# Kernel optimization log

Measured on AMD Instinct MI355X. Metric: run time of the kernel, lower is better.

The kernel has to match this reference:

```python
import jax, jax.numpy as jnp
import numpy as np

H = 12          # num_heads
E = 768         # key_dim
LORA_SCALE = 32.0 / 4.0  # scale / R
NEG = -1e9


def setup_inputs() -> dict:
    key = jax.random.key(0)
    ks = jax.random.split(key, 8)
    B, L = 2, 2048
    return {
        "x": jax.random.normal(ks[0], (B, L, E), jnp.float32),
        "w_in": jax.random.normal(ks[1], (E, 3 * E), jnp.float32) * 0.02,
        "b_in": jnp.zeros((3 * E,), jnp.float32),
        "A_in": jax.random.normal(ks[2], (4, 3 * E), jnp.float32) * 0.02,
        "B_in": jax.random.normal(ks[3], (E, 4), jnp.float32) * 0.02,
        "w_out": jax.random.normal(ks[4], (E, E), jnp.float32) * 0.02,
        "b_out": jnp.zeros((E,), jnp.float32),
        "A_out": jax.random.normal(ks[5], (4, E), jnp.float32) * 0.02,
        "B_out": jax.random.normal(ks[6], (E, 4), jnp.float32) * 0.02,
    }


def reference(x, w_in, b_in, A_in, B_in, w_out, b_out, A_out, B_out):
    Bb, L, _ = x.shape
    D = E // H
    # LoRA-adapted input projection: w + (scale/R) * B @ A
    w1 = w_in + LORA_SCALE * (B_in @ A_in)          # [E, 3E]
    c = jnp.einsum('ble,eo->blo', x, w1) + b_in      # [B, L, 3E]
    q, k, v = jnp.split(c, 3, axis=2)
    # split heads -> [B, H, L, D]
    def heads(t):
        return t.reshape(Bb, L, H, D).transpose(0, 2, 1, 3)
    q, k, v = heads(q), heads(k), heads(v)
    # attention scores (no 1/sqrt(d): scale=False in module defaults)
    w = jnp.einsum('bhqd,bhkd->bhqk', q, k)          # [B, H, L, L]
    band = jnp.tril(jnp.ones((L, L), jnp.float32))   # causal band
    w = w * band + NEG * (1.0 - band)
    w = jax.nn.softmax(w, axis=-1)
    a = jnp.einsum('bhqk,bhkd->bhqd', w, v)          # [B, H, L, D]
    a = a.transpose(0, 2, 1, 3).reshape(Bb, L, E)    # merge heads
    w2 = w_out + LORA_SCALE * (B_out @ A_out)        # [E, E]
    return jnp.einsum('ble,eo->blo', a, w2) + b_out
```

## Files before the change

### kernel.cpp

```cpp
#include <hip/hip_runtime.h>
#include <hip/hip_bf16.h>

#define BB 2
#define LL 2048
#define EE 768
#define HH 12
#define DD 64
#define N3 2304
#define TOK 4096
#define LOG2E 1.4426950408889634f

typedef __attribute__((ext_vector_type(8))) short short8;
typedef __attribute__((ext_vector_type(4))) short s16x4;
typedef __attribute__((ext_vector_type(4))) float f32x4;
typedef __attribute__((ext_vector_type(4))) unsigned int uix4;
typedef unsigned int uint_t;
typedef unsigned short ushort_t;

__device__ __forceinline__ f32x4 mfma16(short8 a, short8 b, f32x4 c) {
  return __builtin_amdgcn_mfma_f32_16x16x32_bf16(a, b, c, 0, 0, 0);
}
__device__ __forceinline__ f32x4 mfma16k16(s16x4 a, s16x4 b, f32x4 c) {
  return __builtin_amdgcn_mfma_f32_16x16x16bf16_1k(a, b, c, 0, 0, 0);
}

__device__ __forceinline__ ushort_t bf16bits(float f) {
  __hip_bfloat16 h = __float2bfloat16(f);
  return *reinterpret_cast<ushort_t*>(&h);
}

__device__ __forceinline__ float bits2f(ushort_t u) {
  union { uint_t u; float f; } cv;
  cv.u = ((uint_t)u) << 16;
  return cv.f;
}

__device__ __forceinline__ void stage64(const __hip_bfloat16* gbase, int ldg,
                                        short* lds, int tid) {
  const int wave = tid >> 6, lane = tid & 63;
#pragma unroll
  for (int c = 0; c < 4; ++c) {
    int off = c * 4096 + wave * 1024 + lane * 16;
    int row = off >> 7;
    int cs  = (off & 127) >> 4;
    int cc  = cs ^ (row & 7);
    __builtin_amdgcn_global_load_lds(
        (const __attribute__((address_space(1))) void*)((const short*)gbase + (size_t)row * ldg + cc * 8),
        (__attribute__((address_space(3))) void*)(lds + c * 2048 + wave * 512),
        16, 0, 0);
  }
}

__device__ __forceinline__ void stage128(const __hip_bfloat16* gbase, int ldg,
                                         short* lds, int tid) {
  const int wave = tid >> 6, lane = tid & 63;
#pragma unroll
  for (int c = 0; c < 4; ++c) {
    int off = c * 4096 + wave * 1024 + lane * 16;
    int row = off >> 8;
    int cs  = (off & 255) >> 4;
    int cc  = cs ^ (row & 7);
    __builtin_amdgcn_global_load_lds(
        (const __attribute__((address_space(1))) void*)((const short*)gbase + (size_t)row * ldg + cc * 8),
        (__attribute__((address_space(3))) void*)(lds + c * 2048 + wave * 512),
        16, 0, 0);
  }
}

__device__ __forceinline__ short8 frag64(const short* lds, int row, int chunk) {
  return *(const short8*)(lds + row * 64 + (chunk ^ (row & 7)) * 8);
}

__global__ void prep_kernel(const float* __restrict__ x, const float* __restrict__ w_in,
                            const float* __restrict__ A_in, const float* __restrict__ B_in,
                            const float* __restrict__ w_out, const float* __restrict__ A_out,
                            const float* __restrict__ B_out,
                            __hip_bfloat16* __restrict__ xb, __hip_bfloat16* __restrict__ w1T,
                            __hip_bfloat16* __restrict__ w2T) {
  __shared__ float tile[32][33];
  const int bid = blockIdx.x, t = threadIdx.x;
  if (bid < 2304) {
    const float *W, *Am, *Bm;
    __hip_bfloat16* out;
    int N, tx, ty;
    if (bid < 1728) { W = w_in;  Am = A_in;  Bm = B_in;  out = w1T; N = N3; tx = bid % 72; ty = bid / 72; }
    else { int jj = bid - 1728; W = w_out; Am = A_out; Bm = B_out; out = w2T; N = EE; tx = jj % 24; ty = jj / 24; }
    const int e0 = ty * 32, o0 = tx * 32;
    const int r = t >> 5, col = t & 31;
#pragma unroll
    for (int i = 0; i < 4; ++i)
      tile[r + i * 8][col] = W[(size_t)(e0 + r + i * 8) * N + (o0 + col)];
    __syncthreads();
    const int e = e0 + col;
    const float b0 = Bm[e * 4 + 0], b1 = Bm[e * 4 + 1], b2 = Bm[e * 4 + 2], b3 = Bm[e * 4 + 3];
#pragma unroll
    for (int i = 0; i < 4; ++i) {
      const int o = o0 + r + i * 8;
      float acc = b0 * Am[o] + b1 * Am[N + o] + b2 * Am[2 * N + o] + b3 * Am[3 * N + o];
      out[(size_t)o * EE + e] = __float2bfloat16(tile[col][r + i * 8] + 8.0f * acc);
    }
  } else {
    const int j = bid - 2304;
    const float* src = x + (size_t)j * 4096 + t * 16;
    short* dst = (short*)xb + (size_t)j * 4096 + t * 16;
#pragma unroll
    for (int half = 0; half < 2; ++half) {
      float4 a = ((const float4*)src)[half * 2];
      float4 b = ((const float4*)src)[half * 2 + 1];
      short8 v;
      v[0] = (short)bf16bits(a.x); v[1] = (short)bf16bits(a.y);
      v[2] = (short)bf16bits(a.z); v[3] = (short)bf16bits(a.w);
      v[4] = (short)bf16bits(b.x); v[5] = (short)bf16bits(b.y);
      v[6] = (short)bf16bits(b.z); v[7] = (short)bf16bits(b.w);
      ((short8*)dst)[half] = v;
    }
  }
}

template<bool F32OUT, bool QSCALE>
__global__ __launch_bounds__(256, 2) void gemm_bt(const __hip_bfloat16* __restrict__ A,
                                                  const __hip_bfloat16* __restrict__ BT,
                                                  const float* __restrict__ bias,
                                                  void* __restrict__ outp,
                                                  int M, int N, int K) {
  __shared__ __align__(16) short Al[128 * 64];
  __shared__ __align__(16) short Bl[128 * 64];
  const int tid = threadIdx.x, lane = tid & 63, wave = tid >> 6;
  const int quad = lane >> 4, c16 = lane & 15;
  const int n0 = blockIdx.x * 128, m0 = blockIdx.y * 128;
  const int msub = (wave & 1) * 64, nsub = (wave >> 1) * 64;
  f32x4 acc[4][4] = {};
  for (int k0 = 0; k0 < K; k0 += 64) {
    __syncthreads();
    stage64(A + (size_t)m0 * K + k0, K, Al, tid);
    stage64(BT + (size_t)n0 * K + k0, K, Bl, tid);
    __syncthreads();
#pragma unroll
    for (int ks = 0; ks < 2; ++ks) {
      short8 af[4], bfr[4];
#pragma unroll
      for (int i = 0; i < 4; ++i) {
        af[i]  = frag64(Al, msub + i * 16 + c16, ks * 4 + quad);
        bfr[i] = frag64(Bl, nsub + i * 16 + c16, ks * 4 + quad);
      }
#pragma unroll
      for (int mi = 0; mi < 4; ++mi)
#pragma unroll
        for (int ni = 0; ni < 4; ++ni)
          acc[mi][ni] = mfma16(af[mi], bfr[ni], acc[mi][ni]);
    }
  }
#pragma unroll
  for (int ni = 0; ni < 4; ++ni) {
    int n = n0 + nsub + ni * 16 + c16;
    float bv = bias[n];
    float sc = (QSCALE && n < EE) ? LOG2E : 1.0f;
#pragma unroll
    for (int mi = 0; mi < 4; ++mi) {
      int row0 = m0 + msub + mi * 16 + quad * 4;
#pragma unroll
      for (int r = 0; r < 4; ++r) {
        float v = (acc[mi][ni][r] + bv) * sc;
        if (F32OUT) ((float*)outp)[(size_t)(row0 + r) * N + n] = v;
        else ((__hip_bfloat16*)outp)[(size_t)(row0 + r) * N + n] = __float2bfloat16(v);
      }
    }
  }
}

__global__ void vtrans_kernel(const __hip_bfloat16* __restrict__ qkv,
                              __hip_bfloat16* __restrict__ vT) {
  const int tid = threadIdx.x, lane = tid & 63, wave = tid >> 6;
  const int blk = blockIdx.x;
  const int bh = blk >> 6, lt = blk & 63;
  const int b = bh / HH, h = bh % HH;
  const int l0 = lt * 32 + wave * 8;
  const int i = lane >> 3, o = lane & 7;
  const short* src = (const short*)qkv + (size_t)(b * LL + l0 + i) * N3 + 2 * EE + h * DD + o * 8;
  uix4 u = *(const uix4*)src;
  {
    uix4 ov;
#pragma unroll
    for (int k = 0; k < 4; ++k) ov[k] = (uint_t)__shfl_xor((int)u[k], 8);
#pragma unroll
    for (int k = 0; k < 4; ++k)
      u[k] = ((i & 1) == 0) ? ((u[k] & 0xFFFFu) | (ov[k] << 16))
                            : ((ov[k] >> 16) | (u[k] & 0xFFFF0000u));
  }
  {
    uix4 ov;
#pragma unroll
    for (int k = 0; k < 4; ++k) ov[k] = (uint_t)__shfl_xor((int)u[k], 16);
    uint_t a0 = ((i & 2) == 0) ? u[0] : ov[1];
    uint_t a1 = ((i & 2) == 0) ? ov[0] : u[1];
    uint_t a2 = ((i & 2) == 0) ? u[2] : ov[3];
    uint_t a3 = ((i & 2) == 0) ? ov[2] : u[3];
    u[0] = a0; u[1] = a1; u[2] = a2; u[3] = a3;
  }
  {
    uix4 ov;
#pragma unroll
    for (int k = 0; k < 4; ++k) ov[k] = (uint_t)__shfl_xor((int)u[k], 32);
    uint_t a0 = ((i & 4) == 0) ? u[0] : ov[2];
    uint_t a1 = ((i & 4) == 0) ? u[1] : ov[3];
    uint_t a2 = ((i & 4) == 0) ? ov[0] : u[2];
    uint_t a3 = ((i & 4) == 0) ? ov[1] : u[3];
    u[0] = a0; u[1] = a1; u[2] = a2; u[3] = a3;
  }
  short* dst = (short*)vT + (size_t)((b * HH + h) * DD + o * 8 + i) * LL + l0;
  *(uix4*)dst = u;
}

#define SLOT_BYTES 16896
union pk4 { uint_t u[2]; s16x4 s4; };

__global__ __launch_bounds__(256, 4) void attn_kernel(const __hip_bfloat16* __restrict__ qkv,
                                                      const __hip_bfloat16* __restrict__ vT,
                                                      char* __restrict__ Opart) {
  __shared__ __align__(16) short Kl[128 * 64];
  __shared__ __align__(16) short Vl[64 * 128];
  const int tid = threadIdx.x, lane = tid & 63, wave = tid >> 6;
  const int quad = lane >> 4, c16 = lane & 15;
  const int bid = blockIdx.x;
  const int bh = bid % 24;
  const int j = bid / 24;
  int qt, cch;
  if (j < 8)       { qt = 8 + j;  cch = 0; }
  else if (j < 16) { qt = 23 - j; cch = 1; }
  else             { qt = 23 - j; cch = 0; }
  const int b = bh / HH, h = bh % HH;
  const int q0 = qt * 128;
  const int qw = q0 + wave * 32;
  const int ks = cch * 1024;
  const int ke = min(q0 + 128, ks + 1024);
  short8 qfA[2], qfB[2];
  {
    const short* qra = (const short*)qkv + (size_t)(b * LL + qw + c16) * N3 + h * DD;
    qfA[0] = *(const short8*)(qra + quad * 8);
    qfA[1] = *(const short8*)(qra + 32 + quad * 8);
    const short* qrb = qra + 16 * N3;
    qfB[0] = *(const short8*)(qrb + quad * 8);
    qfB[1] = *(const short8*)(qrb + 32 + quad * 8);
  }
  float lA = 0.f, lB = 0.f;
  f32x4 oA[4] = {}, oB[4] = {};
  const int vsub = (quad & 1) * 4;
  const int cxor = (c16 & 7);
  for (int k0 = ks; k0 < ke; k0 += 128) {
    __syncthreads();
    stage64(qkv + (size_t)(b * LL + k0) * N3 + EE + h * DD, N3, Kl, tid);
    stage128(vT + (size_t)((b * HH + h) * DD) * LL + k0, LL, Vl, tid);
    __syncthreads();
    int nlimB = (qw + 31 - k0) / 16 + 1; if (nlimB > 8) nlimB = 8;
    int nlimA = (qw + 15 - k0) / 16 + 1; if (nlimA > 8) nlimA = 8;
#pragma unroll
    for (int nt = 0; nt < 8; ++nt) {
      if (nt < nlimB) {
        const short* krow = Kl + (nt * 16 + c16) * 64;
        const int kc0 = (quad ^ cxor) * 8;
        short8 kf0 = *(const short8*)(krow + kc0);
        short8 kf1 = *(const short8*)(krow + (kc0 ^ 32));
        const int kb = k0 + nt * 16 + quad * 4;
        const bool diag = (k0 + nt * 16 + 15 > qw + 16);
        f32x4 sB = {};
        sB = mfma16(kf0, qfB[0], sB);
        sB = mfma16(kf1, qfB[1], sB);
        if (diag) {
          const int q = qw + 16 + c16;
#pragma unroll
          for (int r = 0; r < 4; ++r)
            if (kb + r > q) sB[r] = -1e9f;
        }
        pk4 pB;
        {
          float p0 = exp2f(sB[0]), p1 = exp2f(sB[1]);
          float p2 = exp2f(sB[2]), p3 = exp2f(sB[3]);
          lB += (p0 + p1) + (p2 + p3);
          pB.u[0] = (uint_t)bf16bits(p0) | ((uint_t)bf16bits(p1) << 16);
          pB.u[1] = (uint_t)bf16bits(p2) | ((uint_t)bf16bits(p3) << 16);
        }
        const bool doA = (nt < nlimA);
        pk4 pA;
        if (doA) {
          f32x4 sA = {};
          sA = mfma16(kf0, qfA[0], sA);
          sA = mfma16(kf1, qfA[1], sA);
          if (k0 + nt * 16 + 15 > qw) {
            const int q = qw + c16;
#pragma unroll
            for (int r = 0; r < 4; ++r)
              if (kb + r > q) sA[r] = -1e9f;
          }
          float p0 = exp2f(sA[0]), p1 = exp2f(sA[1]);
          float p2 = exp2f(sA[2]), p3 = exp2f(sA[3]);
          lA += (p0 + p1) + (p2 + p3);
          pA.u[0] = (uint_t)bf16bits(p0) | ((uint_t)bf16bits(p1) << 16);
          pA.u[1] = (uint_t)bf16bits(p2) | ((uint_t)bf16bits(p3) << 16);
        }
        const int cg = nt * 2 + (quad >> 1);
        const short* vbase = Vl + c16 * 128 + ((cg ^ cxor) * 8 + vsub);
#pragma unroll
        for (int dt = 0; dt < 4; ++dt) {
          s16x4 vf = *(const s16x4*)(vbase + dt * 2048);
          oB[dt] = mfma16k16(vf, pB.s4, oB[dt]);
          if (doA) oA[dt] = mfma16k16(vf, pA.s4, oA[dt]);
        }
      }
    }
  }
  lA += __shfl_xor(lA, 16); lA += __shfl_xor(lA, 32);
  lB += __shfl_xor(lB, 16); lB += __shfl_xor(lB, 32);
  char* op = Opart + (size_t)((bh * 16 + qt) * 2 + cch) * SLOT_BYTES;
  float* lout = (float*)(op + 16384);
  __syncthreads();
  if (quad == 0) {
    lout[wave * 32 + c16] = lA;
    lout[wave * 32 + 16 + c16] = lB;
  }
  short* reg = Kl + wave * 1152;
#pragma unroll
  for (int hh = 0; hh < 2; ++hh) {
#pragma unroll
    for (int dt = 0; dt < 4; ++dt) {
      f32x4 o = hh ? oB[dt] : oA[dt];
      uint_t w0 = (uint_t)bf16bits(o[0]) | ((uint_t)bf16bits(o[1]) << 16);
      uint_t w1 = (uint_t)bf16bits(o[2]) | ((uint_t)bf16bits(o[3]) << 16);
      uint_t* p = (uint_t*)(reg + c16 * 72 + dt * 16 + quad * 4);
      p[0] = w0; p[1] = w1;
    }
#pragma unroll
    for (int it = 0; it < 2; ++it) {
      int idx = it * 64 + lane;
      int tq = idx >> 3, c = idx & 7;
      short8 v = *(const short8*)(reg + tq * 72 + c * 8);
      *(short8*)((short*)op + (wave * 32 + hh * 16 + tq) * 64 + c * 8) = v;
    }
  }
}

__global__ void merge_kernel(const char* __restrict__ Opart,
                             __hip_bfloat16* __restrict__ abuf) {
  const int t = threadIdx.x;
  const int bh = blockIdx.x >> 4, qt = blockIdx.x & 15;
  const int b = bh / HH, h = bh % HH;
  const char* p0 = Opart + (size_t)((bh * 16 + qt) * 2) * SLOT_BYTES;
  const char* p1 = p0 + SLOT_BYTES;
  const bool two = (qt >= 8);
  const int q = t >> 1, dc = (t & 1) * 32;
  float l = ((const float*)(p0 + 16384))[q];
  if (two) l += ((const float*)(p1 + 16384))[q];
  const float inv = 1.0f / l;
  const short* o0 = (const short*)p0 + q * 64 + dc;
  const short* o1 = (const short*)p1 + q * 64 + dc;
  __align__(16) short out[32];
#pragma unroll
  for (int blk = 0; blk < 4; ++blk) {
    short8 r0 = *(const short8*)(o0 + blk * 8);
    short8 r1;
    if (two) r1 = *(const short8*)(o1 + blk * 8);
#pragma unroll
    for (int i = 0; i < 8; ++i) {
      float v = bits2f((ushort_t)r0[i]);
      if (two) v += bits2f((ushort_t)r1[i]);
      out[blk * 8 + i] = (short)bf16bits(v * inv);
    }
  }
  short* dst = (short*)abuf + (size_t)(b * LL + qt * 128 + q) * EE + h * DD + dc;
#pragma unroll
  for (int blk = 0; blk < 4; ++blk)
    *(short8*)(dst + blk * 8) = *(short8*)(out + blk * 8);
}

extern "C" void kernel_launch(void* const* d_in, const int* in_sizes, int n_in,
                              void* d_out, int out_size, void* d_ws, size_t ws_size,
                              hipStream_t stream) {
  (void)in_sizes; (void)n_in; (void)out_size; (void)ws_size;
  const float* x     = (const float*)d_in[0];
  const float* w_in  = (const float*)d_in[1];
  const float* b_in  = (const float*)d_in[2];
  const float* A_in  = (const float*)d_in[3];
  const float* B_in  = (const float*)d_in[4];
  const float* w_out = (const float*)d_in[5];
  const float* b_out = (const float*)d_in[6];
  const float* A_out = (const float*)d_in[7];
  const float* B_out = (const float*)d_in[8];
  char* ws = (char*)d_ws;
  __hip_bfloat16* xb   = (__hip_bfloat16*)(ws);
  __hip_bfloat16* w1T  = (__hip_bfloat16*)(ws + 6291456);
  __hip_bfloat16* w2T  = (__hip_bfloat16*)(ws + 9830400);
  __hip_bfloat16* qkv  = (__hip_bfloat16*)(ws + 11010048);
  __hip_bfloat16* vT   = (__hip_bfloat16*)(ws + 29884416);
  __hip_bfloat16* abuf = (__hip_bfloat16*)(ws + 36175872);
  char* Opart          = ws + 42467328;

  prep_kernel<<<3072, 256, 0, stream>>>(x, w_in, A_in, B_in, w_out, A_out, B_out,
                                        xb, w1T, w2T);
  gemm_bt<false, true><<<dim3(N3 / 128, TOK / 128), 256, 0, stream>>>(xb, w1T, b_in, qkv, TOK, N3, EE);
  vtrans_kernel<<<BB * HH * 64, 256, 0, stream>>>(qkv, vT);
  attn_kernel<<<24 * 24, 256, 0, stream>>>(qkv, vT, Opart);
  merge_kernel<<<24 * 16, 256, 0, stream>>>(Opart, abuf);
  gemm_bt<true, false><<<dim3(EE / 128, TOK / 128), 256, 0, stream>>>(abuf, w2T, b_out, d_out, TOK, EE, EE);
}
```

Before: 172.7 us.

## Fuse V transpose into QKV GEMM, double-buffer attention, skip merge for single-chunk tiles

```diff
diff --git a/kernel.cpp b/kernel.cpp
--- a/kernel.cpp
+++ b/kernel.cpp
@@ -27,6 +27,10 @@
 __device__ __forceinline__ ushort_t bf16bits(float f) {
   __hip_bfloat16 h = __float2bfloat16(f);
   return *reinterpret_cast<ushort_t*>(&h);
+}
+
+__device__ __forceinline__ uint_t pack2bf(float a, float b) {
+  return (uint_t)bf16bits(a) | ((uint_t)bf16bits(b) << 16);
 }
 
 __device__ __forceinline__ float bits2f(ushort_t u) {
@@ -117,11 +121,12 @@
   }
 }
 
-template<bool F32OUT, bool QSCALE>
+template<bool F32OUT, bool QSCALE, bool SPLITV>
 __global__ __launch_bounds__(256, 2) void gemm_bt(const __hip_bfloat16* __restrict__ A,
                                                   const __hip_bfloat16* __restrict__ BT,
                                                   const float* __restrict__ bias,
                                                   void* __restrict__ outp,
+                                                  __hip_bfloat16* __restrict__ vTp,
                                                   int M, int N, int K) {
   __shared__ __align__(16) short Al[128 * 64];
   __shared__ __align__(16) short Bl[128 * 64];
@@ -150,6 +155,25 @@
           acc[mi][ni] = mfma16(af[mi], bfr[ni], acc[mi][ni]);
     }
   }
+  if (SPLITV && n0 >= 2 * EE) {
+    const int bofs = (m0 >> 11) * EE;
+    const int l0 = (m0 & 2047) + msub;
+#pragma unroll
+    for (int ni = 0; ni < 4; ++ni) {
+      int n = n0 + nsub + ni * 16 + c16;
+      float bv = bias[n];
+      const size_t rowbase = (size_t)(bofs + (n - 2 * EE)) * LL;
+#pragma unroll
+      for (int mi = 0; mi < 4; ++mi) {
+        int l = l0 + mi * 16 + quad * 4;
+        uint2 w;
+        w.x = pack2bf(acc[mi][ni][0] + bv, acc[mi][ni][1] + bv);
+        w.y = pack2bf(acc[mi][ni][2] + bv, acc[mi][ni][3] + bv);
+        *(uint2*)((short*)vTp + rowbase + l) = w;
+      }
+    }
+    return;
+  }
 #pragma unroll
   for (int ni = 0; ni < 4; ++ni) {
     int n = n0 + nsub + ni * 16 + c16;
@@ -168,57 +192,15 @@
   }
 }
 
-__global__ void vtrans_kernel(const __hip_bfloat16* __restrict__ qkv,
-                              __hip_bfloat16* __restrict__ vT) {
-  const int tid = threadIdx.x, lane = tid & 63, wave = tid >> 6;
-  const int blk = blockIdx.x;
-  const int bh = blk >> 6, lt = blk & 63;
-  const int b = bh / HH, h = bh % HH;
-  const int l0 = lt * 32 + wave * 8;
-  const int i = lane >> 3, o = lane & 7;
-  const short* src = (const short*)qkv + (size_t)(b * LL + l0 + i) * N3 + 2 * EE + h * DD + o * 8;
-  uix4 u = *(const uix4*)src;
-  {
-    uix4 ov;
-#pragma unroll
-    for (int k = 0; k < 4; ++k) ov[k] = (uint_t)__shfl_xor((int)u[k], 8);
-#pragma unroll
-    for (int k = 0; k < 4; ++k)
-      u[k] = ((i & 1) == 0) ? ((u[k] & 0xFFFFu) | (ov[k] << 16))
-                            : ((ov[k] >> 16) | (u[k] & 0xFFFF0000u));
-  }
-  {
-    uix4 ov;
-#pragma unroll
-    for (int k = 0; k < 4; ++k) ov[k] = (uint_t)__shfl_xor((int)u[k], 16);
-    uint_t a0 = ((i & 2) == 0) ? u[0] : ov[1];
-    uint_t a1 = ((i & 2) == 0) ? ov[0] : u[1];
-    uint_t a2 = ((i & 2) == 0) ? u[2] : ov[3];
-    uint_t a3 = ((i & 2) == 0) ? ov[2] : u[3];
-    u[0] = a0; u[1] = a1; u[2] = a2; u[3] = a3;
-  }
-  {
-    uix4 ov;
-#pragma unroll
-    for (int k = 0; k < 4; ++k) ov[k] = (uint_t)__shfl_xor((int)u[k], 32);
-    uint_t a0 = ((i & 4) == 0) ? u[0] : ov[2];
-    uint_t a1 = ((i & 4) == 0) ? u[1] : ov[3];
-    uint_t a2 = ((i & 4) == 0) ? ov[0] : u[2];
-    uint_t a3 = ((i & 4) == 0) ? ov[1] : u[3];
-    u[0] = a0; u[1] = a1; u[2] = a2; u[3] = a3;
-  }
-  short* dst = (short*)vT + (size_t)((b * HH + h) * DD + o * 8 + i) * LL + l0;
-  *(uix4*)dst = u;
-}
-
 #define SLOT_BYTES 16896
 union pk4 { uint_t u[2]; s16x4 s4; };
 
-__global__ __launch_bounds__(256, 4) void attn_kernel(const __hip_bfloat16* __restrict__ qkv,
+__global__ __launch_bounds__(256, 2) void attn_kernel(const __hip_bfloat16* __restrict__ qkv,
                                                       const __hip_bfloat16* __restrict__ vT,
-                                                      char* __restrict__ Opart) {
-  __shared__ __align__(16) short Kl[128 * 64];
-  __shared__ __align__(16) short Vl[64 * 128];
+                                                      char* __restrict__ Opart,
+                                                      __hip_bfloat16* __restrict__ abuf) {
+  __shared__ __align__(16) short Kl[2 * 128 * 64];
+  __shared__ __align__(16) short Vl[2 * 64 * 128];
   const int tid = threadIdx.x, lane = tid & 63, wave = tid >> 6;
   const int quad = lane >> 4, c16 = lane & 15;
   const int bid = blockIdx.x;
@@ -233,6 +215,7 @@
   const int qw = q0 + wave * 32;
   const int ks = cch * 1024;
   const int ke = min(q0 + 128, ks + 1024);
+  const int niter = (ke - ks + 127) >> 7;
   short8 qfA[2], qfB[2];
   {
     const short* qra = (const short*)qkv + (size_t)(b * LL + qw + c16) * N3 + h * DD;
@@ -246,17 +229,27 @@
   f32x4 oA[4] = {}, oB[4] = {};
   const int vsub = (quad & 1) * 4;
   const int cxor = (c16 & 7);
-  for (int k0 = ks; k0 < ke; k0 += 128) {
+  const __hip_bfloat16* kgbase = qkv + (size_t)(b * LL) * N3 + EE + h * DD;
+  const __hip_bfloat16* vgbase = vT + (size_t)((b * HH + h) * DD) * LL;
+  stage64(kgbase + (size_t)ks * N3, N3, Kl, tid);
+  stage128(vgbase + ks, LL, Vl, tid);
+  for (int it = 0; it < niter; ++it) {
+    const int k0 = ks + it * 128;
     __syncthreads();
-    stage64(qkv + (size_t)(b * LL + k0) * N3 + EE + h * DD, N3, Kl, tid);
-    stage128(vT + (size_t)((b * HH + h) * DD) * LL + k0, LL, Vl, tid);
-    __syncthreads();
+    if (it + 1 < niter) {
+      short* Kn = Kl + ((it + 1) & 1) * 8192;
+      short* Vn = Vl + ((it + 1) & 1) * 8192;
+      stage64(kgbase + (size_t)(k0 + 128) * N3, N3, Kn, tid);
+      stage128(vgbase + k0 + 128, LL, Vn, tid);
+    }
+    const short* Kb = Kl + (it & 1) * 8192;
+    const short* Vb = Vl + (it & 1) * 8192;
     int nlimB = (qw + 31 - k0) / 16 + 1; if (nlimB > 8) nlimB = 8;
     int nlimA = (qw + 15 - k0) / 16 + 1; if (nlimA > 8) nlimA = 8;
 #pragma unroll
     for (int nt = 0; nt < 8; ++nt) {
       if (nt < nlimB) {
-        const short* krow = Kl + (nt * 16 + c16) * 64;
+        const short* krow = Kb + (nt * 16 + c16) * 64;
         const int kc0 = (quad ^ cxor) * 8;
         short8 kf0 = *(const short8*)(krow + kc0);
         short8 kf1 = *(const short8*)(krow + (kc0 ^ 32));
@@ -276,8 +269,8 @@
           float p0 = exp2f(sB[0]), p1 = exp2f(sB[1]);
           float p2 = exp2f(sB[2]), p3 = exp2f(sB[3]);
           lB += (p0 + p1) + (p2 + p3);
-          pB.u[0] = (uint_t)bf16bits(p0) | ((uint_t)bf16bits(p1) << 16);
-          pB.u[1] = (uint_t)bf16bits(p2) | ((uint_t)bf16bits(p3) << 16);
+          pB.u[0] = pack2bf(p0, p1);
+          pB.u[1] = pack2bf(p2, p3);
         }
         const bool doA = (nt < nlimA);
         pk4 pA;
@@ -294,11 +287,11 @@
           float p0 = exp2f(sA[0]), p1 = exp2f(sA[1]);
           float p2 = exp2f(sA[2]), p3 = exp2f(sA[3]);
           lA += (p0 + p1) + (p2 + p3);
-          pA.u[0] = (uint_t)bf16bits(p0) | ((uint_t)bf16bits(p1) << 16);
-          pA.u[1] = (uint_t)bf16bits(p2) | ((uint_t)bf16bits(p3) << 16);
+          pA.u[0] = pack2bf(p0, p1);
+          pA.u[1] = pack2bf(p2, p3);
         }
         const int cg = nt * 2 + (quad >> 1);
-        const short* vbase = Vl + c16 * 128 + ((cg ^ cxor) * 8 + vsub);
+        const short* vbase = Vb + c16 * 128 + ((cg ^ cxor) * 8 + vsub);
 #pragma unroll
         for (int dt = 0; dt < 4; ++dt) {
           s16x4 vf = *(const s16x4*)(vbase + dt * 2048);
@@ -310,30 +303,36 @@
   }
   lA += __shfl_xor(lA, 16); lA += __shfl_xor(lA, 32);
   lB += __shfl_xor(lB, 16); lB += __shfl_xor(lB, 32);
+  const bool single = (cch == 0) && (qt < 8);
+  const float nA = single ? 1.0f / lA : 1.0f;
+  const float nB = single ? 1.0f / lB : 1.0f;
   char* op = Opart + (size_t)((bh * 16 + qt) * 2 + cch) * SLOT_BYTES;
-  float* lout = (float*)(op + 16384);
   __syncthreads();
-  if (quad == 0) {
+  if (!single && quad == 0) {
+    float* lout = (float*)(op + 16384);
     lout[wave * 32 + c16] = lA;
     lout[wave * 32 + 16 + c16] = lB;
   }
   short* reg = Kl + wave * 1152;
 #pragma unroll
   for (int hh = 0; hh < 2; ++hh) {
+    const float sc = hh ? nB : nA;
 #pragma unroll
     for (int dt = 0; dt < 4; ++dt) {
       f32x4 o = hh ? oB[dt] : oA[dt];
-      uint_t w0 = (uint_t)bf16bits(o[0]) | ((uint_t)bf16bits(o[1]) << 16);
-      uint_t w1 = (uint_t)bf16bits(o[2]) | ((uint_t)bf16bits(o[3]) << 16);
       uint_t* p = (uint_t*)(reg + c16 * 72 + dt * 16 + quad * 4);
-      p[0] = w0; p[1] = w1;
+      p[0] = pack2bf(o[0] * sc, o[1] * sc);
+      p[1] = pack2bf(o[2] * sc, o[3] * sc);
     }
 #pragma unroll
     for (int it = 0; it < 2; ++it) {
       int idx = it * 64 + lane;
       int tq = idx >> 3, c = idx & 7;
       short8 v = *(const short8*)(reg + tq * 72 + c * 8);
-      *(short8*)((short*)op + (wave * 32 + hh * 16 + tq) * 64 + c * 8) = v;
+      if (single)
+        *(short8*)((short*)abuf + (size_t)(b * LL + q0 + wave * 32 + hh * 16 + tq) * EE + h * DD + c * 8) = v;
+      else
+        *(short8*)((short*)op + (wave * 32 + hh * 16 + tq) * 64 + c * 8) = v;
     }
   }
 }
@@ -341,14 +340,12 @@
 __global__ void merge_kernel(const char* __restrict__ Opart,
                              __hip_bfloat16* __restrict__ abuf) {
   const int t = threadIdx.x;
-  const int bh = blockIdx.x >> 4, qt = blockIdx.x & 15;
+  const int bh = blockIdx.x >> 3, qt = 8 + (blockIdx.x & 7);
   const int b = bh / HH, h = bh % HH;
   const char* p0 = Opart + (size_t)((bh * 16 + qt) * 2) * SLOT_BYTES;
   const char* p1 = p0 + SLOT_BYTES;
-  const bool two = (qt >= 8);
   const int q = t >> 1, dc = (t & 1) * 32;
-  float l = ((const float*)(p0 + 16384))[q];
-  if (two) l += ((const float*)(p1 + 16384))[q];
+  float l = ((const float*)(p0 + 16384))[q] + ((const float*)(p1 + 16384))[q];
   const float inv = 1.0f / l;
   const short* o0 = (const short*)p0 + q * 64 + dc;
   const short* o1 = (const short*)p1 + q * 64 + dc;
@@ -356,12 +353,10 @@
 #pragma unroll
   for (int blk = 0; blk < 4; ++blk) {
     short8 r0 = *(const short8*)(o0 + blk * 8);
-    short8 r1;
-    if (two) r1 = *(const short8*)(o1 + blk * 8);
+    short8 r1 = *(const short8*)(o1 + blk * 8);
 #pragma unroll
     for (int i = 0; i < 8; ++i) {
-      float v = bits2f((ushort_t)r0[i]);
-      if (two) v += bits2f((ushort_t)r1[i]);
+      float v = bits2f((ushort_t)r0[i]) + bits2f((ushort_t)r1[i]);
       out[blk * 8 + i] = (short)bf16bits(v * inv);
     }
   }
@@ -395,9 +390,10 @@
 
   prep_kernel<<<3072, 256, 0, stream>>>(x, w_in, A_in, B_in, w_out, A_out, B_out,
                                         xb, w1T, w2T);
-  gemm_bt<false, true><<<dim3(N3 / 128, TOK / 128), 256, 0, stream>>>(xb, w1T, b_in, qkv, TOK, N3, EE);
-  vtrans_kernel<<<BB * HH * 64, 256, 0, stream>>>(qkv, vT);
-  attn_kernel<<<24 * 24, 256, 0, stream>>>(qkv, vT, Opart);
-  merge_kernel<<<24 * 16, 256, 0, stream>>>(Opart, abuf);
-  gemm_bt<true, false><<<dim3(EE / 128, TOK / 128), 256, 0, stream>>>(abuf, w2T, b_out, d_out, TOK, EE, EE);
-}
+  gemm_bt<false, true, true><<<dim3(N3 / 128, TOK / 128), 256, 0, stream>>>(
+      xb, w1T, b_in, qkv, vT, TOK, N3, EE);
+  attn_kernel<<<24 * 24, 256, 0, stream>>>(qkv, vT, Opart, abuf);
+  merge_kernel<<<24 * 8, 256, 0, stream>>>(Opart, abuf);
+  gemm_bt<true, false, false><<<dim3(EE / 128, TOK / 128), 256, 0, stream>>>(
+      abuf, w2T, b_out, d_out, nullptr, TOK, EE, EE);
+}
```

New measurement: 169.6 us. About the same (-1.7%).
